# Performance work log

Measured on AMD Instinct MI355X. Metric: run time of the kernel, lower is better.

The kernel has to match this reference:

```python
import jax, jax.numpy as jnp
import numpy as np

B, T, C, H = 4, 2048, 1024, 16
HS = C // H  # head_size = 64
EPS = 1e-5


def setup_inputs() -> dict:
    key = jax.random.key(0)
    ks = jax.random.split(key, 16)
    s = 0.02
    inp = {
        "x": jax.random.normal(ks[0], (B, T, C), jnp.float32),
        # custom LayerNorm buffers (gamma=ones, beta=zeros in source)
        "ln1_g": jnp.ones((C,), jnp.float32),
        "ln1_b": jnp.zeros((C,), jnp.float32),
        "ln2_g": jnp.ones((C,), jnp.float32),
        "ln2_b": jnp.zeros((C,), jnp.float32),
        # per-head Q/K/V linears, stacked over heads: [H, C, HS]
        "Wq": jax.random.normal(ks[1], (H, C, HS), jnp.float32) * s,
        "bq": jax.random.normal(ks[2], (H, HS), jnp.float32) * s,
        "Wk": jax.random.normal(ks[3], (H, C, HS), jnp.float32) * s,
        "bk": jax.random.normal(ks[4], (H, HS), jnp.float32) * s,
        "Wv": jax.random.normal(ks[5], (H, C, HS), jnp.float32) * s,
        "bv": jax.random.normal(ks[6], (H, HS), jnp.float32) * s,
        # output projection [C, C]
        "Wo": jax.random.normal(ks[7], (C, C), jnp.float32) * s,
        "bo": jax.random.normal(ks[8], (C,), jnp.float32) * s,
        # FFN: C -> 4C -> C
        "W1": jax.random.normal(ks[9], (C, 4 * C), jnp.float32) * s,
        "b1": jax.random.normal(ks[10], (4 * C,), jnp.float32) * s,
        "W2": jax.random.normal(ks[11], (4 * C, C), jnp.float32) * s,
        "b2": jax.random.normal(ks[12], (C,), jnp.float32) * s,
    }
    return inp


def _layernorm_time_axis(x, g, b):
    # Faithful to source: normalizes over axis=1 (time), unbiased variance (ddof=1).
    m = jnp.mean(x, axis=1, keepdims=True)
    v = jnp.var(x, axis=1, keepdims=True, ddof=1)
    return g * (x - m) / jnp.sqrt(v + EPS) + b


def reference(x, ln1_g, ln1_b, ln2_g, ln2_b, Wq, bq, Wk, bk, Wv, bv, Wo, bo, W1, b1, W2, b2):
    Bc, Tc, Cc = x.shape
    h = _layernorm_time_axis(x, ln1_g, ln1_b)
    # per-head projections: [B, H, T, HS]
    q = jnp.einsum('btc,hcd->bhtd', h, Wq) + bq[None, :, None, :]
    k = jnp.einsum('btc,hcd->bhtd', h, Wk) + bk[None, :, None, :]
    v = jnp.einsum('btc,hcd->bhtd', h, Wv) + bv[None, :, None, :]
    # scores scaled by C**-0.5 (full embed dim, as in source)
    wei = jnp.einsum('bhtd,bhsd->bhts', q, k) * (Cc ** -0.5)
    causal = jnp.tril(jnp.ones((Tc, Tc), bool))
    wei = jnp.where(causal[None, None], wei, -jnp.inf)
    wei = jax.nn.softmax(wei, axis=-1)
    att = jnp.einsum('bhts,bhsd->bhtd', wei, v)
    # concat heads -> [B, T, C], then projection
    att = att.transpose(0, 2, 1, 3).reshape(Bc, Tc, Cc)
    x = x + att @ Wo + bo
    # FFN on ln2
    h2 = _layernorm_time_axis(x, ln2_g, ln2_b)
    ff = jax.nn.relu(h2 @ W1 + b1) @ W2 + b2
    return x + ff
```

## Files before the change

### kernel.cpp

```cpp
#include <hip/hip_runtime.h>

#define B_   4
#define T_   2048
#define C_   1024
#define H_   16
#define HS_  64
#define BT_  (B_*T_)
#define EPS_ 1e-5f

typedef unsigned short u16;
typedef unsigned int   u32;
typedef __attribute__((ext_vector_type(8))) __bf16 bf16x8;
typedef __attribute__((ext_vector_type(4))) float  f32x4;
typedef __attribute__((ext_vector_type(8))) u16    u16x8;
typedef __attribute__((ext_vector_type(4))) u16    u16x4;
typedef __attribute__((ext_vector_type(4))) u32    u32x4;

__device__ __forceinline__ u16 f2bf(float f) {
  unsigned x = __builtin_bit_cast(unsigned, f);
  x += 0x7fffu + ((x >> 16) & 1u);
  return (u16)(x >> 16);
}
__device__ __forceinline__ float bf2f(u16 v) {
  return __builtin_bit_cast(float, (u32)v << 16);
}

__device__ __forceinline__ float fast_exp2(float x) {
  float y;
  asm("v_exp_f32 %0, %1" : "=v"(y) : "v"(x));
  return y;
}
__device__ __forceinline__ float fast_rcp(float x) {
  float y;
  asm("v_rcp_f32 %0, %1" : "=v"(y) : "v"(x));
  return y;
}

#define GLD_LDS16(src, dst) \
  __builtin_amdgcn_global_load_lds((__attribute__((address_space(1))) void*)(src), \
                                   (__attribute__((address_space(3))) void*)(dst), 16, 0, 0)

__global__ __launch_bounds__(256) void ln_partial(const float* __restrict__ x,
                                                  float* __restrict__ ps,
                                                  float* __restrict__ psq) {
  int col = blockIdx.x * 256 + threadIdx.x;
  int b = col >> 10, c = col & (C_ - 1);
  int t0 = blockIdx.y * (T_ / 16);
  const float* p = x + (size_t)b * T_ * C_ + (size_t)t0 * C_ + c;
  float s = 0.f, sq = 0.f;
  #pragma unroll 4
  for (int i = 0; i < T_ / 16; ++i) { float v = p[(size_t)i * C_]; s += v; sq += v * v; }
  ps [blockIdx.y * (B_ * C_) + col] = s;
  psq[blockIdx.y * (B_ * C_) + col] = sq;
}

__global__ __launch_bounds__(256) void ln_partial_bf(const u16* __restrict__ x,
                                                     float* __restrict__ ps,
                                                     float* __restrict__ psq) {
  int col = blockIdx.x * 256 + threadIdx.x;
  int b = col >> 10, c = col & (C_ - 1);
  int t0 = blockIdx.y * (T_ / 16);
  const u16* p = x + (size_t)b * T_ * C_ + (size_t)t0 * C_ + c;
  float s = 0.f, sq = 0.f;
  #pragma unroll 4
  for (int i = 0; i < T_ / 16; ++i) { float v = bf2f(p[(size_t)i * C_]); s += v; sq += v * v; }
  ps [blockIdx.y * (B_ * C_) + col] = s;
  psq[blockIdx.y * (B_ * C_) + col] = sq;
}

__global__ __launch_bounds__(256) void ln_final(const float* __restrict__ ps,
                                                const float* __restrict__ psq,
                                                float* __restrict__ mean,
                                                float* __restrict__ rstd) {
  int col = blockIdx.x * 256 + threadIdx.x;
  float s = 0.f, sq = 0.f;
  #pragma unroll
  for (int i = 0; i < 16; ++i) { s += ps[i * (B_ * C_) + col]; sq += psq[i * (B_ * C_) + col]; }
  float m = s * (1.f / T_);
  float var = (sq - (float)T_ * m * m) * (1.f / (T_ - 1));
  mean[col] = m;
  rstd[col] = rsqrtf(var + EPS_);
}

__global__ __launch_bounds__(256) void ln_norm(const float* __restrict__ x,
                                               const float* __restrict__ mean,
                                               const float* __restrict__ rstd,
                                               const float* __restrict__ gam,
                                               const float* __restrict__ bet,
                                               u16* __restrict__ out) {
  size_t i = ((size_t)blockIdx.x * 256 + threadIdx.x) * 4;
  int c  = (int)(i & (C_ - 1));
  int b  = (int)(i >> 21);
  int bc = (b << 10) + c;
  float4 v = *(const float4*)(x + i);
  float vv[4] = {v.x, v.y, v.z, v.w};
  u16x4 o;
  #pragma unroll
  for (int j = 0; j < 4; ++j)
    o[j] = f2bf(gam[c + j] * (vv[j] - mean[bc + j]) * rstd[bc + j] + bet[c + j]);
  *(u16x4*)(out + i) = o;
}

__global__ __launch_bounds__(256) void ln_norm_bf(const u16* __restrict__ x,
                                                  const float* __restrict__ mean,
                                                  const float* __restrict__ rstd,
                                                  const float* __restrict__ gam,
                                                  const float* __restrict__ bet,
                                                  u16* __restrict__ out) {
  size_t i = ((size_t)blockIdx.x * 256 + threadIdx.x) * 4;
  int c  = (int)(i & (C_ - 1));
  int b  = (int)(i >> 21);
  int bc = (b << 10) + c;
  u16x4 v = *(const u16x4*)(x + i);
  u16x4 o;
  #pragma unroll
  for (int j = 0; j < 4; ++j)
    o[j] = f2bf(gam[c + j] * (bf2f(v[j]) - mean[bc + j]) * rstd[bc + j] + bet[c + j]);
  *(u16x4*)(out + i) = o;
}

__global__ __launch_bounds__(256) void transpose_cast(const float* __restrict__ in,
                                                      u16* __restrict__ out,
                                                      int cols_in, int ld_out,
                                                      size_t batch_in, size_t batch_out) {
  __shared__ float tile[32][33];
  const float* I = in + (size_t)blockIdx.z * batch_in;
  u16* Ou = out + (size_t)blockIdx.z * batch_out;
  int r0 = blockIdx.y << 5, c0 = blockIdx.x << 5;
  int tx = threadIdx.x & 31, ty = threadIdx.x >> 5;
  #pragma unroll
  for (int rr = 0; rr < 32; rr += 8)
    tile[ty + rr][tx] = I[(size_t)(r0 + ty + rr) * cols_in + c0 + tx];
  __syncthreads();
  #pragma unroll
  for (int rr = 0; rr < 32; rr += 8)
    Ou[(size_t)(c0 + ty + rr) * ld_out + r0 + tx] = f2bf(tile[tx][ty + rr]);
}

__global__ __launch_bounds__(256) void concat_bias(const float* __restrict__ bq,
                                                   const float* __restrict__ bk,
                                                   const float* __restrict__ bv,
                                                   float* __restrict__ out) {
  int i = blockIdx.x * 256 + threadIdx.x;
  float v = (i < 1024) ? bq[i] : (i < 2048 ? bk[i - 1024] : bv[i - 2048]);
  out[i] = v;
}

__global__ __launch_bounds__(256) void v_transpose(const u16* __restrict__ qkv,
                                                   u16* __restrict__ Vt) {
  __shared__ u16 tile[32][33];
  int bh = blockIdx.z; int b = bh >> 4, h = bh & 15;
  int t0 = blockIdx.x << 5, hs0 = blockIdx.y << 5;
  int tx = threadIdx.x & 31, ty = threadIdx.x >> 5;
  const u16* src = qkv + (size_t)(b * T_ + t0) * 3072 + 2048 + h * 64 + hs0;
  #pragma unroll
  for (int rr = 0; rr < 32; rr += 8)
    tile[ty + rr][tx] = src[(size_t)(ty + rr) * 3072 + tx];
  __syncthreads();
  u16* dst = Vt + ((size_t)bh * 64 + hs0) * T_ + t0;
  #pragma unroll
  for (int rr = 0; rr < 32; rr += 8)
    dst[(size_t)(ty + rr) * T_ + tx] = tile[tx][ty + rr];
}

template<int RELU, int QSCALE>
__global__ __launch_bounds__(256, 2)
void gemm_128x256(const u16* __restrict__ A,
                  const u16* __restrict__ Bt,
                  const float* __restrict__ bias,
                  u16* __restrict__ outp,
                  int M, int N, int K) {
  constexpr int BK = 32;
  __shared__ u16 sA[3][128 * BK];
  __shared__ u16 sB[3][256 * BK];

  const int tid = threadIdx.x;
  const int wave = tid >> 6, lane = tid & 63;
  const int g = lane >> 4, r16 = lane & 15;

  const int nbx = N >> 8;
  const int nwg = gridDim.x;
  const int bid = blockIdx.x;
  const int swz = ((bid & 7) * (nwg >> 3)) + (bid >> 3);
  const int bx = swz % nbx, by = swz / nbx;
  const int row0 = by << 7, col0 = bx << 8;

  const u16* aS[2];
  const u16* bS[4];
  #pragma unroll
  for (int j = 0; j < 2; ++j) {
    const int ci = tid + 256 * j, row = ci >> 2, cc = ci & 3;
    aS[j] = A + (size_t)(row0 + row) * K + ((cc ^ ((row >> 1) & 3)) * 8);
  }
  #pragma unroll
  for (int j = 0; j < 4; ++j) {
    const int ci = tid + 256 * j, row = ci >> 2, cc = ci & 3;
    bS[j] = Bt + (size_t)(col0 + row) * K + ((cc ^ ((row >> 1) & 3)) * 8);
  }
  const int ldsOff = wave * 512;

  auto stage = [&](int t, int buf) {
    const int ko = t * BK;
    #pragma unroll
    for (int j = 0; j < 2; ++j)
      GLD_LDS16(aS[j] + ko, &sA[buf][ldsOff + j * 2048]);
    #pragma unroll
    for (int j = 0; j < 4; ++j)
      GLD_LDS16(bS[j] + ko, &sB[buf][ldsOff + j * 2048]);
  };

  const int wrow = (wave >> 1) * 64;
  const int wcol = (wave & 1) * 128;
  f32x4 acc[4][8] = {};

  const int NT = K / BK;

  stage(0, 0); stage(1, 1);
  asm volatile("s_waitcnt vmcnt(6)" ::: "memory");
  __builtin_amdgcn_s_barrier();
  __builtin_amdgcn_sched_barrier(0);

  for (int t = 0; t < NT; ++t) {
    const u16* As = sA[t % 3];
    const u16* Bs = sB[t % 3];
    bf16x8 af[4], bf[8];
    #pragma unroll
    for (int m = 0; m < 4; ++m) {
      const int lr = wrow + m * 16 + r16;
      af[m] = *(const bf16x8*)&As[lr * 32 + ((g ^ ((lr >> 1) & 3)) * 8)];
    }
    #pragma unroll
    for (int n = 0; n < 8; ++n) {
      const int lr = wcol + n * 16 + r16;
      bf[n] = *(const bf16x8*)&Bs[lr * 32 + ((g ^ ((lr >> 1) & 3)) * 8)];
    }
    if (t + 2 < NT) stage(t + 2, (t + 2) % 3);

    __builtin_amdgcn_s_setprio(1);
    #pragma unroll
    for (int m = 0; m < 4; ++m)
      #pragma unroll
      for (int n = 0; n < 8; ++n)
        acc[m][n] = __builtin_amdgcn_mfma_f32_16x16x32_bf16(af[m], bf[n], acc[m][n], 0, 0, 0);
    __builtin_amdgcn_s_setprio(0);

    if (t + 1 < NT) {
      if (t + 2 < NT) asm volatile("s_waitcnt vmcnt(6)" ::: "memory");
      else            asm volatile("s_waitcnt vmcnt(0)" ::: "memory");
      __builtin_amdgcn_s_barrier();
      __builtin_amdgcn_sched_barrier(0);
    }
  }

  #pragma unroll
  for (int m = 0; m < 4; ++m) {
    #pragma unroll
    for (int n = 0; n < 8; ++n) {
      const int col = col0 + wcol + n * 16 + r16;
      const float bv = bias[col];
      const float sc = (QSCALE && col < 1024) ? 0.04508422003f : 1.f;
      const int rowb = row0 + wrow + m * 16 + g * 4;
      #pragma unroll
      for (int r = 0; r < 4; ++r) {
        float v = acc[m][n][r] + bv;
        if (RELU) v = fmaxf(v, 0.f);
        if (QSCALE) v *= sc;
        outp[(size_t)(rowb + r) * N + col] = f2bf(v);
      }
    }
  }
}

template<int RELU, int RAW, int QSCALE>
__global__ __launch_bounds__(512, 2)
void gemm_256(const u16* __restrict__ A,
              const u16* __restrict__ Bt,
              const float* __restrict__ bias,
              void* __restrict__ outp,
              void* __restrict__ outp_b,
              int M, int N, int K) {
  constexpr int BK = 32;
  __shared__ u16 sA[4][256 * BK];
  __shared__ u16 sB[4][256 * BK];

  const int tid = threadIdx.x;
  const int wave = tid >> 6, lane = tid & 63;
  const int g = lane >> 4, r16 = lane & 15;

  const int nbx = N >> 8;
  const int nwg = gridDim.x;
  const int bid = blockIdx.x;
  const int swz = ((bid & 7) * (nwg >> 3)) + (bid >> 3);
  const int bx = swz % nbx, by = swz / nbx;
  const int row0 = by << 8, col0 = bx << 8;

  const int kspan = RAW ? (K >> 1) : K;
  const int kbase = RAW ? ((int)blockIdx.y * kspan) : 0;

  const u16* aS[2];
  const u16* bS[2];
  #pragma unroll
  for (int j = 0; j < 2; ++j) {
    const int ci = tid + 512 * j, row = ci >> 2, cc = ci & 3;
    aS[j] = A  + (size_t)(row0 + row) * K + ((cc ^ ((row >> 1) & 3)) * 8) + kbase;
    bS[j] = Bt + (size_t)(col0 + row) * K + ((cc ^ ((row >> 1) & 3)) * 8) + kbase;
  }
  const int ldsOff = wave * 512;

  auto stage = [&](int t, int buf) {
    const int ko = t * BK;
    #pragma unroll
    for (int j = 0; j < 2; ++j)
      GLD_LDS16(aS[j] + ko, &sA[buf][ldsOff + j * 4096]);
    #pragma unroll
    for (int j = 0; j < 2; ++j)
      GLD_LDS16(bS[j] + ko, &sB[buf][ldsOff + j * 4096]);
  };

  const int wrow = (wave >> 2) * 128;
  const int wcol = (wave & 3) * 64;
  f32x4 acc[8][4] = {};

  const int NT = kspan / BK;

  stage(0, 0); stage(1, 1);
  asm volatile("s_waitcnt vmcnt(4)" ::: "memory");
  __builtin_amdgcn_s_barrier();
  __builtin_amdgcn_sched_barrier(0);

  for (int t = 0; t < NT; ++t) {
    const u16* As = sA[t & 3];
    const u16* Bs = sB[t & 3];
    bf16x8 af[8], bf[4];
    #pragma unroll
    for (int m = 0; m < 8; ++m) {
      const int lr = wrow + m * 16 + r16;
      af[m] = *(const bf16x8*)&As[lr * 32 + ((g ^ ((lr >> 1) & 3)) * 8)];
    }
    #pragma unroll
    for (int n = 0; n < 4; ++n) {
      const int lr = wcol + n * 16 + r16;
      bf[n] = *(const bf16x8*)&Bs[lr * 32 + ((g ^ ((lr >> 1) & 3)) * 8)];
    }
    if (t + 2 < NT) stage(t + 2, (t + 2) & 3);

    __builtin_amdgcn_s_setprio(1);
    #pragma unroll
    for (int m = 0; m < 8; ++m)
      #pragma unroll
      for (int n = 0; n < 4; ++n)
        acc[m][n] = __builtin_amdgcn_mfma_f32_16x16x32_bf16(af[m], bf[n], acc[m][n], 0, 0, 0);
    __builtin_amdgcn_s_setprio(0);

    if (t + 1 < NT) {
      if (t + 2 < NT) asm volatile("s_waitcnt vmcnt(4)" ::: "memory");
      else            asm volatile("s_waitcnt vmcnt(0)" ::: "memory");
      __builtin_amdgcn_s_barrier();
      __builtin_amdgcn_sched_barrier(0);
    }
  }

  if constexpr (RAW) {
    float* po = blockIdx.y ? (float*)outp_b : (float*)outp;
    #pragma unroll
    for (int m = 0; m < 8; ++m) {
      #pragma unroll
      for (int n = 0; n < 4; ++n) {
        const int col = col0 + wcol + n * 16 + r16;
        const int rowb = row0 + wrow + m * 16 + g * 4;
        #pragma unroll
        for (int r = 0; r < 4; ++r)
          po[(size_t)(rowb + r) * N + col] = acc[m][n][r];
      }
    }
  } else {
    u16* po = (u16*)outp;
    #pragma unroll
    for (int m = 0; m < 8; ++m) {
      #pragma unroll
      for (int n = 0; n < 4; ++n) {
        const int col = col0 + wcol + n * 16 + r16;
        const float bv = bias[col];
        const float sc = (QSCALE && col < 1024) ? 0.04508422003f : 1.f;
        const int rowb = row0 + wrow + m * 16 + g * 4;
        #pragma unroll
        for (int r = 0; r < 4; ++r) {
          float v = acc[m][n][r] + bv;
          if (RELU) v = fmaxf(v, 0.f);
          if (QSCALE) v *= sc;
          po[(size_t)(rowb + r) * N + col] = f2bf(v);
        }
      }
    }
  }
}

__global__ __launch_bounds__(256) void ffn2_reduce(const float* __restrict__ pA,
                                                   const u16* __restrict__ res,
                                                   const float* __restrict__ bias,
                                                   float* __restrict__ out) {
  size_t i = ((size_t)blockIdx.x * 256 + threadIdx.x) * 4;
  float4 a = *(const float4*)(pA + i);
  float4 o = *(const float4*)(out + i);
  u16x4 r = *(const u16x4*)(res + i);
  const int c = (int)(i & (C_ - 1));
  float4 bb = *(const float4*)(bias + c);
  float4 v;
  v.x = a.x + o.x + bf2f(r[0]) + bb.x;
  v.y = a.y + o.y + bf2f(r[1]) + bb.y;
  v.z = a.z + o.z + bf2f(r[2]) + bb.z;
  v.w = a.w + o.w + bf2f(r[3]) + bb.w;
  *(float4*)(out + i) = v;
}

template<int BM, int BN, int THREADS, int OUT_F32, int RELU, int RES>
__global__ __launch_bounds__(THREADS, 3)
void gemm_pipe(const u16* __restrict__ A,
               const u16* __restrict__ Bt,
               const float* __restrict__ bias,
               const float* __restrict__ res,
               void* __restrict__ outp,
               int M, int N, int K) {
  constexpr int BK  = 32;
  constexpr int CHA = (BM * 4) / THREADS;
  constexpr int CHB = (BN * 4) / THREADS;
  constexpr int CH  = CHA + CHB;

  __shared__ u16 sA[3][BM * BK];
  __shared__ u16 sB[3][BN * BK];

  const int tid = threadIdx.x;
  const int wave = tid >> 6, lane = tid & 63;
  const int g = lane >> 4, r16 = lane & 15;

  const int nbx = N / BN;
  const int nwg = gridDim.x;
  const int bid = blockIdx.x;
  const int swz = ((bid & 7) * (nwg >> 3)) + (bid >> 3);
  const int bx = swz % nbx, by = swz / nbx;
  const int row0 = by * BM, col0 = bx * BN;

  const u16* aS[CHA];
  const u16* bS[CHB];
  #pragma unroll
  for (int j = 0; j < CHA; ++j) {
    const int ci = tid + THREADS * j, row = ci >> 2, cc = ci & 3;
    aS[j] = A + (size_t)(row0 + row) * K + ((cc ^ ((row >> 1) & 3)) * 8);
  }
  #pragma unroll
  for (int j = 0; j < CHB; ++j) {
    const int ci = tid + THREADS * j, row = ci >> 2, cc = ci & 3;
    bS[j] = Bt + (size_t)(col0 + row) * K + ((cc ^ ((row >> 1) & 3)) * 8);
  }
  const int ldsOff = wave * 512;

  auto stage = [&](int t, int buf) {
    const int ko = t * BK;
    #pragma unroll
    for (int j = 0; j < CHA; ++j)
      GLD_LDS16(aS[j] + ko, &sA[buf][ldsOff + j * (THREADS * 8)]);
    #pragma unroll
    for (int j = 0; j < CHB; ++j)
      GLD_LDS16(bS[j] + ko, &sB[buf][ldsOff + j * (THREADS * 8)]);
  };

  const int wrow = (wave >> 1) * 64;
  const int wcol = (wave & 1) * 64;
  f32x4 acc[4][4] = {};

  const int NT = K / BK;

  stage(0, 0); stage(1, 1);
  if constexpr (CH == 3) asm volatile("s_waitcnt vmcnt(3)" ::: "memory");
  else                   asm volatile("s_waitcnt vmcnt(4)" ::: "memory");
  __builtin_amdgcn_s_barrier();
  __builtin_amdgcn_sched_barrier(0);

  for (int t = 0; t < NT; ++t) {
    if (t + 2 < NT) stage(t + 2, (t + 2) % 3);
    const u16* As = sA[t % 3];
    const u16* Bs = sB[t % 3];
    bf16x8 af[4], bf[4];
    #pragma unroll
    for (int m = 0; m < 4; ++m) {
      const int lr = wrow + m * 16 + r16;
      af[m] = *(const bf16x8*)&As[lr * 32 + ((g ^ ((lr >> 1) & 3)) * 8)];
    }
    #pragma unroll
    for (int n = 0; n < 4; ++n) {
      const int lr = wcol + n * 16 + r16;
      bf[n] = *(const bf16x8*)&Bs[lr * 32 + ((g ^ ((lr >> 1) & 3)) * 8)];
    }
    __builtin_amdgcn_s_setprio(1);
    #pragma unroll
    for (int m = 0; m < 4; ++m)
      #pragma unroll
      for (int n = 0; n < 4; ++n)
        acc[m][n] = __builtin_amdgcn_mfma_f32_16x16x32_bf16(af[m], bf[n], acc[m][n], 0, 0, 0);
    __builtin_amdgcn_s_setprio(0);

    if (t + 1 < NT) {
      if (t + 2 < NT) {
        if constexpr (CH == 3) asm volatile("s_waitcnt vmcnt(3)" ::: "memory");
        else                   asm volatile("s_waitcnt vmcnt(4)" ::: "memory");
      } else {
        asm volatile("s_waitcnt vmcnt(0)" ::: "memory");
      }
      __builtin_amdgcn_s_barrier();
      __builtin_amdgcn_sched_barrier(0);
    }
  }

  #pragma unroll
  for (int m = 0; m < 4; ++m) {
    #pragma unroll
    for (int n = 0; n < 4; ++n) {
      const int col = col0 + wcol + n * 16 + r16;
      const float bv = bias[col];
      const int rowb = row0 + wrow + m * 16 + g * 4;
      #pragma unroll
      for (int r = 0; r < 4; ++r) {
        const size_t idx = (size_t)(rowb + r) * N + col;
        float v = acc[m][n][r] + bv;
        if (RES)  v += res[idx];
        if (RELU) v = fmaxf(v, 0.f);
        if (OUT_F32) ((float*)outp)[idx] = v;
        else         ((u16*)outp)[idx]   = f2bf(v);
      }
    }
  }
}

__global__ __launch_bounds__(256) void attn_fwd(const u16* __restrict__ qkv,
                                                const u16* __restrict__ Vt,
                                                u16* __restrict__ O) {
  __shared__ u16 sK[3][64 * 64];
  __shared__ u16 sV[3][64 * 64];

  const int orig = blockIdx.x;
  const int work = ((orig & 7) << 7) + (orig >> 3);
  const int i = work & 15;
  const int h = (work >> 4) & 15;
  const int b = work >> 8;
  const int qA = i << 6, qB = (31 - i) << 6;
  const int nA = i + 1,  nB = 32 - i;

  const int tid = threadIdx.x, wave = tid >> 6, lane = tid & 63;
  const int g = lane >> 4, r16 = lane & 15;

  const size_t base = (size_t)b * T_ * 3072 + h * 64;
  const u16* Qp = qkv + base;
  const u16* Kp = qkv + base + 1024;
  const u16* VtP = Vt + (size_t)(b * 16 + h) * 64 * T_;

  const int rowL = lane >> 3;
  const int colL = 8 * ((lane & 7) ^ rowL);
  const u16* kSrc = Kp  + (size_t)(wave * 16 + rowL) * 3072 + colL;
  const u16* vSrc = VtP + (size_t)(wave * 16 + rowL) * T_   + colL;
  u16* kDst0 = &sK[0][(wave * 16 + 0) * 64];
  u16* kDst8 = &sK[0][(wave * 16 + 8) * 64];
  u16* vDst0 = &sV[0][(wave * 16 + 0) * 64];
  u16* vDst8 = &sV[0][(wave * 16 + 8) * 64];

  const int ck0 = (( 0 + g * 16) ^ ((r16 & 7) << 4)) >> 1;
  const int ck1 = ((64 + g * 16) ^ ((r16 & 7) << 4)) >> 1;

  bf16x8 qfA[2], qfB[2];
  #pragma unroll
  for (int kc = 0; kc < 2; ++kc) {
    qfA[kc] = *(const bf16x8*)(Qp + (size_t)(qA + wave * 16 + r16) * 3072 + kc * 32 + g * 8);
    qfB[kc] = *(const bf16x8*)(Qp + (size_t)(qB + wave * 16 + r16) * 3072 + kc * 32 + g * 8);
  }

  f32x4 accA[4] = {}, accB[4] = {};
  f32x4 lA4 = {}, lB4 = {};
  const int qaA = qA + wave * 16 + r16;
  const int qaB = qB + wave * 16 + r16;

  const u32 one2 = 0x3F803F80u;
  const u32x4 onesv = {one2, one2, one2, one2};
  const bf16x8 ONES = __builtin_bit_cast(bf16x8, onesv);

  int sbuf = 0;
  auto stageAdv = [&]() {
    const int o = sbuf * 4096;
    GLD_LDS16(kSrc,            kDst0 + o);
    GLD_LDS16(kSrc + 8 * 3072, kDst8 + o);
    GLD_LDS16(vSrc,            vDst0 + o);
    GLD_LDS16(vSrc + 8 * T_,   vDst8 + o);
    kSrc += 64 * 3072;
    vSrc += 64;
    sbuf = (sbuf == 2) ? 0 : sbuf + 1;
  };

  auto qkt = [&](const bf16x8* kf0, const bf16x8* kf1, const bf16x8* qf, f32x4* s) {
    __builtin_amdgcn_s_setprio(1);
    #pragma unroll
    for (int ni = 0; ni < 4; ++ni) {
      f32x4 t = {};
      t = __builtin_amdgcn_mfma_f32_16x16x32_bf16(kf0[ni], qf[0], t, 0, 0, 0);
      t = __builtin_amdgcn_mfma_f32_16x16x32_bf16(kf1[ni], qf[1], t, 0, 0, 0);
      s[ni] = t;
    }
    __builtin_amdgcn_s_setprio(0);
  };

  auto softmax_pack = [&](f32x4* s, bool diag, int q_abs, int kv0, bf16x8* pa) {
    if (diag) {
      #pragma unroll
      for (int ni = 0; ni < 4; ++ni)
        #pragma unroll
        for (int r = 0; r < 4; ++r) {
          const int kv_abs = kv0 + ni * 16 + g * 4 + r;
          if (kv_abs > q_abs) s[ni][r] = -3e38f;
        }
    }
    #pragma unroll
    for (int ni = 0; ni < 4; ++ni)
      #pragma unroll
      for (int r = 0; r < 4; ++r)
        s[ni][r] = fast_exp2(s[ni][r]);

    u32 pk[4][2];
    #pragma unroll
    for (int ni = 0; ni < 4; ++ni)
      #pragma unroll
      for (int h2 = 0; h2 < 2; ++h2)
        asm("v_cvt_pk_bf16_f32 %0, %1, %2"
            : "=v"(pk[ni][h2]) : "v"(s[ni][2 * h2]), "v"(s[ni][2 * h2 + 1]));

    u32 pa32[2][4];
    #pragma unroll
    for (int kc = 0; kc < 2; ++kc)
      #pragma unroll
      for (int h2 = 0; h2 < 2; ++h2) {
        u32 a = pk[2 * kc][h2], bq_ = pk[2 * kc + 1][h2];
        asm("v_permlane32_swap_b32 %0, %1" : "+v"(a), "+v"(bq_));
        asm("v_permlane16_swap_b32 %0, %1" : "+v"(a), "+v"(bq_));
        pa32[kc][h2] = a;
        pa32[kc][2 + h2] = bq_;
      }
    #pragma unroll
    for (int kc = 0; kc < 2; ++kc) {
      u32x4 tmp = {pa32[kc][0], pa32[kc][1], pa32[kc][2], pa32[kc][3]};
      pa[kc] = __builtin_bit_cast(bf16x8, tmp);
    }
  };

  stageAdv();
  stageAdv();
  asm volatile("s_waitcnt vmcnt(4)" ::: "memory");
  __builtin_amdgcn_s_barrier();
  __builtin_amdgcn_sched_barrier(0);

  int cbuf = 0;
  for (int t = 0; t < nB; ++t) {
    if (t + 2 < nB) stageAdv();
    const u16* Kb = sK[cbuf];
    const u16* Vb = sV[cbuf];
    const int kv0 = t << 6;
    const bool actA = (t < nA);

    bf16x8 kf0[4], kf1[4];
    #pragma unroll
    for (int ni = 0; ni < 4; ++ni) {
      kf0[ni] = *(const bf16x8*)&Kb[(ni * 16 + r16) * 64 + ck0];
      kf1[ni] = *(const bf16x8*)&Kb[(ni * 16 + r16) * 64 + ck1];
    }

    f32x4 s[4];
    bf16x8 paB[2], paA[2];

    qkt(kf0, kf1, qfB, s);
    softmax_pack(s, t == nB - 1, qaB, kv0, paB);
    if (actA) {
      qkt(kf0, kf1, qfA, s);
      softmax_pack(s, t == nA - 1, qaA, kv0, paA);
    }

    bf16x8 vf0[4], vf1[4];
    #pragma unroll
    for (int hsb = 0; hsb < 4; ++hsb) {
      vf0[hsb] = *(const bf16x8*)&Vb[(hsb * 16 + r16) * 64 + ck0];
      vf1[hsb] = *(const bf16x8*)&Vb[(hsb * 16 + r16) * 64 + ck1];
    }

    __builtin_amdgcn_s_setprio(1);
    lB4 = __builtin_amdgcn_mfma_f32_16x16x32_bf16(paB[0], ONES, lB4, 0, 0, 0);
    lB4 = __builtin_amdgcn_mfma_f32_16x16x32_bf16(paB[1], ONES, lB4, 0, 0, 0);
    #pragma unroll
    for (int hsb = 0; hsb < 4; ++hsb) {
      accB[hsb] = __builtin_amdgcn_mfma_f32_16x16x32_bf16(paB[0], vf0[hsb], accB[hsb], 0, 0, 0);
      accB[hsb] = __builtin_amdgcn_mfma_f32_16x16x32_bf16(paB[1], vf1[hsb], accB[hsb], 0, 0, 0);
    }
    if (actA) {
      lA4 = __builtin_amdgcn_mfma_f32_16x16x32_bf16(paA[0], ONES, lA4, 0, 0, 0);
      lA4 = __builtin_amdgcn_mfma_f32_16x16x32_bf16(paA[1], ONES, lA4, 0, 0, 0);
      #pragma unroll
      for (int hsb = 0; hsb < 4; ++hsb) {
        accA[hsb] = __builtin_amdgcn_mfma_f32_16x16x32_bf16(paA[0], vf0[hsb], accA[hsb], 0, 0, 0);
        accA[hsb] = __builtin_amdgcn_mfma_f32_16x16x32_bf16(paA[1], vf1[hsb], accA[hsb], 0, 0, 0);
      }
    }
    __builtin_amdgcn_s_setprio(0);

    if (t + 1 < nB) {
      if (t + 2 < nB) asm volatile("s_waitcnt vmcnt(4)" ::: "memory");
      else            asm volatile("s_waitcnt vmcnt(0)" ::: "memory");
      __builtin_amdgcn_s_barrier();
      __builtin_amdgcn_sched_barrier(0);
    }
    cbuf = (cbuf == 2) ? 0 : cbuf + 1;
  }

  float rlA[4], rlB[4];
  #pragma unroll
  for (int r = 0; r < 4; ++r) {
    rlA[r] = fast_rcp(lA4[r]);
    rlB[r] = fast_rcp(lB4[r]);
  }
  #pragma unroll
  for (int hsb = 0; hsb < 4; ++hsb)
    #pragma unroll
    for (int r = 0; r < 4; ++r) {
      const size_t rowA = (size_t)b * T_ + qA + wave * 16 + g * 4 + r;
      const size_t rowB = (size_t)b * T_ + qB + wave * 16 + g * 4 + r;
      O[rowA * C_ + h * 64 + hsb * 16 + r16] = f2bf(accA[hsb][r] * rlA[r]);
      O[rowB * C_ + h * 64 + hsb * 16 + r16] = f2bf(accB[hsb][r] * rlB[r]);
    }
}

extern "C" void kernel_launch(void* const* d_in, const int* in_sizes, int n_in,
                              void* d_out, int out_size, void* d_ws, size_t ws_size,
                              hipStream_t stream) {
  const float* x    = (const float*)d_in[0];
  const float* ln1g = (const float*)d_in[1];
  const float* ln1b = (const float*)d_in[2];
  const float* ln2g = (const float*)d_in[3];
  const float* ln2b = (const float*)d_in[4];
  const float* Wq   = (const float*)d_in[5];
  const float* bq   = (const float*)d_in[6];
  const float* Wk   = (const float*)d_in[7];
  const float* bk   = (const float*)d_in[8];
  const float* Wv   = (const float*)d_in[9];
  const float* bv   = (const float*)d_in[10];
  const float* Wo   = (const float*)d_in[11];
  const float* bo   = (const float*)d_in[12];
  const float* W1   = (const float*)d_in[13];
  const float* b1   = (const float*)d_in[14];
  const float* W2   = (const float*)d_in[15];
  const float* b2   = (const float*)d_in[16];

  char* w = (char*)d_ws;
  float* ps    = (float*)(w + 0);
  float* psq   = (float*)(w + 262144);
  float* mean  = (float*)(w + 524288);
  float* rstd  = (float*)(w + 540672);
  float* bqkv  = (float*)(w + 557056);
  u16*   h     = (u16*)  (w + 573440);
  u16*   wqkvT = (u16*)  (w + 17350656);
  u16*   woT   = (u16*)  (w + 23642112);
  u16*   w1T   = (u16*)  (w + 25739264);
  u16*   w2T   = (u16*)  (w + 34127872);
  u16*   x1b   = (u16*)  (w + 42516480);
  u16*   Vt    = (u16*)  (w + 59293696);
  u16*   qkv   = (u16*)  (w + 76070912);
  u16*   Oo    = (u16*)  (w + 126402560);
  u16*   u     = qkv;
  float* pA    = (float*)(w + 573440);

  transpose_cast<<<dim3(2, 32, 16), 256, 0, stream>>>(Wq, wqkvT,                     64,   1024, (size_t)C_ * 64, (size_t)64 * 1024);
  transpose_cast<<<dim3(2, 32, 16), 256, 0, stream>>>(Wk, wqkvT + (size_t)1024*1024, 64,   1024, (size_t)C_ * 64, (size_t)64 * 1024);
  transpose_cast<<<dim3(2, 32, 16), 256, 0, stream>>>(Wv, wqkvT + (size_t)2048*1024, 64,   1024, (size_t)C_ * 64, (size_t)64 * 1024);
  transpose_cast<<<dim3(32, 32, 1), 256, 0, stream>>>(Wo, woT, 1024, 1024, 0, 0);
  transpose_cast<<<dim3(128, 32, 1), 256, 0, stream>>>(W1, w1T, 4096, 1024, 0, 0);
  transpose_cast<<<dim3(32, 128, 1), 256, 0, stream>>>(W2, w2T, 1024, 4096, 0, 0);
  concat_bias<<<12, 256, 0, stream>>>(bq, bk, bv, bqkv);

  ln_partial<<<dim3(16, 16), 256, 0, stream>>>(x, ps, psq);
  ln_final<<<16, 256, 0, stream>>>(ps, psq, mean, rstd);
  ln_norm<<<8192, 256, 0, stream>>>(x, mean, rstd, ln1g, ln1b, h);

  gemm_128x256<0, 1><<<768, 256, 0, stream>>>(h, wqkvT, bqkv, qkv, BT_, 3072, 1024);

  v_transpose<<<dim3(T_ / 32, 2, B_ * H_), 256, 0, stream>>>(qkv, Vt);

  attn_fwd<<<1024, 256, 0, stream>>>(qkv, Vt, Oo);

  gemm_pipe<128, 128, 256, 0, 0, 1><<<512, 256, 0, stream>>>(Oo, woT, bo, x, x1b, BT_, 1024, 1024);

  ln_partial_bf<<<dim3(16, 16), 256, 0, stream>>>(x1b, ps, psq);
  ln_final<<<16, 256, 0, stream>>>(ps, psq, mean, rstd);
  ln_norm_bf<<<8192, 256, 0, stream>>>(x1b, mean, rstd, ln2g, ln2b, h);

  gemm_128x256<1, 0><<<1024, 256, 0, stream>>>(h, w1T, b1, u, BT_, 4096, 1024);
  gemm_256<0, 1, 0><<<dim3(128, 2), 512, 0, stream>>>(u, w2T, nullptr, pA, d_out, BT_, 1024, 4096);
  ffn2_reduce<<<8192, 256, 0, stream>>>(pA, x1b, b2, (float*)d_out);
}
```

Before: 402.9 us.

## Double-buffer attention K/V staging and fold FFN2 bias/residual into GEMM epilogue

The attention kernel drops from triple- to double-buffered K/V shared memory, with full vmcnt(0) waits, and declares launch bounds of 4 blocks per CU. The goal is more resident blocks per CU, at the cost of less prefetch depth and more exposed load latency. Separately, the bias and bf16 residual add for the FFN2 output move into the second split-K half's epilogue, so the reduce kernel reads fewer inputs. That epilogue now does extra scattered residual loads.

```diff
diff --git a/kernel.cpp b/kernel.cpp
--- a/kernel.cpp
+++ b/kernel.cpp
@@ -276,6 +276,7 @@
 void gemm_256(const u16* __restrict__ A,
               const u16* __restrict__ Bt,
               const float* __restrict__ bias,
+              const u16* __restrict__ resb,
               void* __restrict__ outp,
               void* __restrict__ outp_b,
               int M, int N, int K) {
@@ -361,16 +362,34 @@
   }
 
   if constexpr (RAW) {
-    float* po = blockIdx.y ? (float*)outp_b : (float*)outp;
-    #pragma unroll
-    for (int m = 0; m < 8; ++m) {
-      #pragma unroll
-      for (int n = 0; n < 4; ++n) {
-        const int col = col0 + wcol + n * 16 + r16;
-        const int rowb = row0 + wrow + m * 16 + g * 4;
+    if (blockIdx.y) {
+      float* po = (float*)outp_b;
+      #pragma unroll
+      for (int m = 0; m < 8; ++m) {
         #pragma unroll
-        for (int r = 0; r < 4; ++r)
-          po[(size_t)(rowb + r) * N + col] = acc[m][n][r];
+        for (int n = 0; n < 4; ++n) {
+          const int col = col0 + wcol + n * 16 + r16;
+          const float bv = bias[col];
+          const int rowb = row0 + wrow + m * 16 + g * 4;
+          #pragma unroll
+          for (int r = 0; r < 4; ++r) {
+            const size_t idx = (size_t)(rowb + r) * N + col;
+            po[idx] = acc[m][n][r] + bv + bf2f(resb[idx]);
+          }
+        }
+      }
+    } else {
+      float* po = (float*)outp;
+      #pragma unroll
+      for (int m = 0; m < 8; ++m) {
+        #pragma unroll
+        for (int n = 0; n < 4; ++n) {
+          const int col = col0 + wcol + n * 16 + r16;
+          const int rowb = row0 + wrow + m * 16 + g * 4;
+          #pragma unroll
+          for (int r = 0; r < 4; ++r)
+            po[(size_t)(rowb + r) * N + col] = acc[m][n][r];
+        }
       }
     }
   } else {
@@ -396,20 +415,15 @@
 }
 
 __global__ __launch_bounds__(256) void ffn2_reduce(const float* __restrict__ pA,
-                                                   const u16* __restrict__ res,
-                                                   const float* __restrict__ bias,
                                                    float* __restrict__ out) {
   size_t i = ((size_t)blockIdx.x * 256 + threadIdx.x) * 4;
   float4 a = *(const float4*)(pA + i);
   float4 o = *(const float4*)(out + i);
-  u16x4 r = *(const u16x4*)(res + i);
-  const int c = (int)(i & (C_ - 1));
-  float4 bb = *(const float4*)(bias + c);
   float4 v;
-  v.x = a.x + o.x + bf2f(r[0]) + bb.x;
-  v.y = a.y + o.y + bf2f(r[1]) + bb.y;
-  v.z = a.z + o.z + bf2f(r[2]) + bb.z;
-  v.w = a.w + o.w + bf2f(r[3]) + bb.w;
+  v.x = a.x + o.x;
+  v.y = a.y + o.y;
+  v.z = a.z + o.z;
+  v.w = a.w + o.w;
   *(float4*)(out + i) = v;
 }
 
@@ -531,11 +545,11 @@
   }
 }
 
-__global__ __launch_bounds__(256) void attn_fwd(const u16* __restrict__ qkv,
-                                                const u16* __restrict__ Vt,
-                                                u16* __restrict__ O) {
-  __shared__ u16 sK[3][64 * 64];
-  __shared__ u16 sV[3][64 * 64];
+__global__ __launch_bounds__(256, 4) void attn_fwd(const u16* __restrict__ qkv,
+                                                   const u16* __restrict__ Vt,
+                                                   u16* __restrict__ O) {
+  __shared__ u16 sK[2][64 * 64];
+  __shared__ u16 sV[2][64 * 64];
 
   const int orig = blockIdx.x;
   const int work = ((orig & 7) << 7) + (orig >> 3);
@@ -590,7 +604,7 @@
     GLD_LDS16(vSrc + 8 * T_,   vDst8 + o);
     kSrc += 64 * 3072;
     vSrc += 64;
-    sbuf = (sbuf == 2) ? 0 : sbuf + 1;
+    sbuf ^= 1;
   };
 
   auto qkt = [&](const bf16x8* kf0, const bf16x8* kf1, const bf16x8* qf, f32x4* s) {
@@ -648,14 +662,13 @@
   };
 
   stageAdv();
-  stageAdv();
-  asm volatile("s_waitcnt vmcnt(4)" ::: "memory");
+  asm volatile("s_waitcnt vmcnt(0)" ::: "memory");
   __builtin_amdgcn_s_barrier();
   __builtin_amdgcn_sched_barrier(0);
 
   int cbuf = 0;
   for (int t = 0; t < nB; ++t) {
-    if (t + 2 < nB) stageAdv();
+    if (t + 1 < nB) stageAdv();
     const u16* Kb = sK[cbuf];
     const u16* Vb = sV[cbuf];
     const int kv0 = t << 6;
@@ -705,12 +718,11 @@
     __builtin_amdgcn_s_setprio(0);
 
     if (t + 1 < nB) {
-      if (t + 2 < nB) asm volatile("s_waitcnt vmcnt(4)" ::: "memory");
-      else            asm volatile("s_waitcnt vmcnt(0)" ::: "memory");
+      asm volatile("s_waitcnt vmcnt(0)" ::: "memory");
       __builtin_amdgcn_s_barrier();
       __builtin_amdgcn_sched_barrier(0);
     }
-    cbuf = (cbuf == 2) ? 0 : cbuf + 1;
+    cbuf ^= 1;
   }
 
   float rlA[4], rlB[4];
@@ -794,6 +806,6 @@
   ln_norm_bf<<<8192, 256, 0, stream>>>(x1b, mean, rstd, ln2g, ln2b, h);
 
   gemm_128x256<1, 0><<<1024, 256, 0, stream>>>(h, w1T, b1, u, BT_, 4096, 1024);
-  gemm_256<0, 1, 0><<<dim3(128, 2), 512, 0, stream>>>(u, w2T, nullptr, pA, d_out, BT_, 1024, 4096);
-  ffn2_reduce<<<8192, 256, 0, stream>>>(pA, x1b, b2, (float*)d_out);
-}
+  gemm_256<0, 1, 0><<<dim3(128, 2), 512, 0, stream>>>(u, w2T, b2, x1b, pA, d_out, BT_, 1024, 4096);
+  ffn2_reduce<<<8192, 256, 0, stream>>>(pA, (float*)d_out);
+}
```

New measurement: 394.5 us. 1.02x faster.
